# Kernel tuning notes

Measured on AMD Instinct MI355X. Metric: run time of the kernel, lower is better.

The kernel has to match this reference:

```python
import jax, jax.numpy as jnp
import numpy as np

K = 5            # neighbors
TEMP = 1.0       # softmax temperature
BANK = 1000      # fixed bank capacity in source
B = 65536        # batch
D = 256          # feature_dim
EPS = 1e-12      # F.normalize eps


def _l2norm(x):
    # F.normalize(x, dim=1): x / max(||x||, eps)
    n = jnp.sqrt(jnp.sum(x * x, axis=1, keepdims=True))
    return x / jnp.maximum(n, EPS)


def setup_inputs() -> dict:
    key = jax.random.key(0)
    k1, k2, k3, k4 = jax.random.split(key, 4)
    features = jax.random.normal(k1, (B, D), dtype=jnp.float32)
    feature_bank = jax.random.normal(k2, (BANK, D), dtype=jnp.float32)
    # fusion_layer: Linear(2D -> D), ReLU, Linear(D -> D). torch weight layout [out, in].
    W1 = jax.random.normal(k3, (D, 2 * D), dtype=jnp.float32) * (1.0 / np.sqrt(2 * D))
    b1 = jnp.zeros((D,), dtype=jnp.float32)
    W2 = jax.random.normal(k4, (D, D), dtype=jnp.float32) * (1.0 / np.sqrt(D))
    b2 = jnp.zeros((D,), dtype=jnp.float32)
    return {"features": features, "feature_bank": feature_bank,
            "W1": W1, "b1": b1, "W2": W2, "b2": b2}


def reference(features, feature_bank, W1, b1, W2, b2):
    # knn_search: cosine similarity against the (full) bank
    qn = _l2norm(features)                      # [B, D]
    bn = _l2norm(feature_bank)                  # [BANK, D]
    sims = qn @ bn.T                            # [B, BANK]
    top_s, top_i = jax.lax.top_k(sims, K)       # [B, K]
    w = jax.nn.softmax(top_s / TEMP, axis=1)    # [B, K]
    neigh = feature_bank[top_i]                 # gather -> [B, K, D]
    nf = jnp.einsum('bkd,bk->bd', neigh, w)     # weighted average of neighbors
    # fusion MLP on concat([query, neighbors])
    fused = jnp.concatenate([features, nf], axis=1)    # [B, 2D]
    h = jax.nn.relu(fused @ W1.T + b1)                 # [B, D]
    out = h @ W2.T + b2                                # [B, D]
    return out
```

## Files before the change

### kernel.cpp

```cpp
#include <hip/hip_runtime.h>

#define DIM 256
#define NC 12

typedef __attribute__((ext_vector_type(8))) short short8;
typedef __attribute__((ext_vector_type(4))) float f32x4;

__device__ __forceinline__ short f32bf(float f) {
    unsigned u = __builtin_bit_cast(unsigned, f);
    unsigned r = u + 0x7FFFu + ((u >> 16) & 1u);
    return (short)(r >> 16);
}

__device__ __forceinline__ void gld_lds16(const void* g, void* l) {
    __builtin_amdgcn_global_load_lds((const __attribute__((address_space(1))) unsigned int*)g,
                                     (__attribute__((address_space(3))) unsigned int*)l, 16, 0, 0);
}

template<int CTRL>
__device__ __forceinline__ unsigned dppmax(unsigned x) {
    unsigned y = (unsigned)__builtin_amdgcn_update_dpp(0, (int)x, CTRL, 0xF, 0xF, true);
    return x > y ? x : y;
}

__global__ __launch_bounds__(256) void k_prep(const float* __restrict__ bank,
        const float* __restrict__ W1, const float* __restrict__ W2,
        short* __restrict__ bnbf, double* __restrict__ binv,
        short* __restrict__ w1bf, short* __restrict__ w2bf)
{
    __shared__ double part[4];
    __shared__ double s_inv;
    const int bid = blockIdx.x, t = threadIdx.x;
    if (bid < 1024) {
        const int row = bid;
        if (row < 1000) {
            float v = bank[(size_t)row * DIM + t];
            double ssq = (double)v * (double)v;
            for (int o = 32; o > 0; o >>= 1) ssq += __shfl_down(ssq, o);
            if ((t & 63) == 0) part[t >> 6] = ssq;
            __syncthreads();
            if (t == 0) {
                double s = part[0] + part[1] + part[2] + part[3];
                double n = sqrt(s); if (n < 1e-12) n = 1e-12;
                double inv = 1.0 / n;
                binv[row] = inv; s_inv = inv;
            }
            __syncthreads();
            const int pcol = (((t >> 3) ^ (row & 7)) << 3) | (t & 7);
            bnbf[(size_t)row * DIM + pcol] = f32bf((float)((double)v * s_inv));
        } else {
            bnbf[(size_t)row * DIM + t] = 0;
            if (t == 0) binv[row] = 0.0;
        }
    } else if (bid < 1536) {
        const int i = (bid - 1024) * 256 + t;
        w1bf[i] = f32bf(W1[i]);
    } else {
        const int i = (bid - 1536) * 256 + t;
        w2bf[i] = f32bf(W2[i]);
    }
}

__global__ __launch_bounds__(256) void k_sims(const float* __restrict__ feat,
        const short* __restrict__ bnbf, short* __restrict__ sims, int qoff)
{
    __shared__ alignas(16) short Qs[32 * 264];
    __shared__ alignas(16) short Ab[64 * 256];
    const int t = threadIdx.x, lane = t & 63, w = t >> 6;
    const int n16 = lane & 15, q4 = lane >> 4;

    {
        const int r = t >> 3, p = t & 7;
        const float4* src = (const float4*)(feat + (size_t)(qoff + blockIdx.x * 32 + r) * DIM + p * 32);
        short* dst = Qs + r * 264 + p * 32;
        #pragma unroll
        for (int i = 0; i < 8; ++i) {
            float4 v = src[i];
            dst[i*4+0] = f32bf(v.x); dst[i*4+1] = f32bf(v.y);
            dst[i*4+2] = f32bf(v.z); dst[i*4+3] = f32bf(v.w);
        }
    }
    const char* gA = (const char*)bnbf;
    char* lA = (char*)Ab;
    #pragma unroll
    for (int i = 0; i < 8; ++i)
        gld_lds16(gA + i * 4096 + t * 16, lA + i * 4096 + (t >> 6) * 1024);
    __syncthreads();

    short8 bq[8][2];
    #pragma unroll
    for (int kc = 0; kc < 8; ++kc)
        #pragma unroll
        for (int nt = 0; nt < 2; ++nt)
            bq[kc][nt] = *(const short8*)(Qs + (nt * 16 + n16) * 264 + kc * 32 + q4 * 8);

    const int ml = w * 16 + n16;
    int aoff[8];
    #pragma unroll
    for (int kc = 0; kc < 8; ++kc)
        aoff[kc] = (ml * 256 + (((kc * 4 + q4) ^ (ml & 7)) << 3)) * 2;

    const f32x4 vzero = {0.f, 0.f, 0.f, 0.f};
    for (int chunk = 0; chunk < 16; ++chunk) {
        f32x4 acc[2];
        acc[0] = vzero; acc[1] = vzero;
        #pragma unroll
        for (int kc = 0; kc < 8; ++kc) {
            short8 af = *(const short8*)(lA + aoff[kc]);
            #pragma unroll
            for (int nt = 0; nt < 2; ++nt)
                acc[nt] = __builtin_amdgcn_mfma_f32_16x16x32_bf16(af, bq[kc][nt], acc[nt], 0, 0, 0);
        }
        const int bankb = chunk * 64 + w * 16 + q4 * 4;
        #pragma unroll
        for (int nt = 0; nt < 2; ++nt) {
            const int qc = blockIdx.x * 32 + nt * 16 + n16;
            uint2 u;
            u.x = ((unsigned)(unsigned short)f32bf(acc[nt][0])) |
                  (((unsigned)(unsigned short)f32bf(acc[nt][1])) << 16);
            u.y = ((unsigned)(unsigned short)f32bf(acc[nt][2])) |
                  (((unsigned)(unsigned short)f32bf(acc[nt][3])) << 16);
            *(uint2*)(sims + (size_t)qc * 1024 + bankb) = u;
        }
        __syncthreads();
        if (chunk < 15) {
            #pragma unroll
            for (int i = 0; i < 8; ++i)
                gld_lds16(gA + (size_t)(chunk + 1) * 32768 + i * 4096 + t * 16,
                          lA + i * 4096 + (t >> 6) * 1024);
            __syncthreads();
        }
    }
}

__global__ __launch_bounds__(256) void k_select(const short* __restrict__ sims,
        int* __restrict__ top, int qoff)
{
    const int t = threadIdx.x, lane = t & 63, w = t >> 6;
    const int q = blockIdx.x * 4 + w;
    const uint4* p = (const uint4*)(sims + (size_t)q * 1024 + lane * 16);
    uint4 a = p[0], b = p[1];

    unsigned k[16];
    {
        unsigned words[8] = {a.x, a.y, a.z, a.w, b.x, b.y, b.z, b.w};
        #pragma unroll
        for (int j = 0; j < 16; ++j) {
            unsigned h = (j & 1) ? (words[j >> 1] >> 16) : (words[j >> 1] & 0xFFFFu);
            unsigned m = (h ^ 0x8000u) ^ ((0u - (h >> 15)) & 0x7FFFu);
            int idx = lane * 16 + j;
            k[j] = (idx < 1000) ? ((m << 16) | (unsigned)idx) : 0u;
        }
    }
    #pragma unroll
    for (int sz = 2; sz <= 16; sz <<= 1)
        #pragma unroll
        for (int st = sz >> 1; st >= 1; st >>= 1)
            #pragma unroll
            for (int i = 0; i < 16; ++i) {
                int j = i ^ st;
                if (j > i) {
                    bool desc = ((i & sz) == 0);
                    unsigned lo = k[i], hi = k[j];
                    unsigned mx = lo > hi ? lo : hi;
                    unsigned mn = lo > hi ? hi : lo;
                    k[i] = desc ? mx : mn;
                    k[j] = desc ? mn : mx;
                }
            }
    unsigned mine = 0;
    #pragma unroll
    for (int r = 0; r < 12; ++r) {
        unsigned m = k[0];
        m = dppmax<0xB1>(m);
        m = dppmax<0x4E>(m);
        m = dppmax<0x141>(m);
        m = dppmax<0x140>(m);
        m = dppmax<0x142>(m);
        m = dppmax<0x143>(m);
        unsigned wm = (unsigned)__builtin_amdgcn_readlane((int)m, 63);
        if (lane == r) mine = wm;
        if (k[0] == wm) {
            #pragma unroll
            for (int s = 0; s < 12; ++s) k[s] = k[s + 1];
        }
    }
    if (lane < 12) top[(size_t)(qoff + q) * NC + lane] = (int)(mine & 0xFFFFu);
}

__global__ __launch_bounds__(256) void k_refine(const float* __restrict__ feat,
        const float* __restrict__ bank, const int* __restrict__ top,
        const double* __restrict__ binv, short* __restrict__ nf)
{
    __shared__ int    cidxL[16 * NC];
    __shared__ float  bdF[16 * NC];
    __shared__ double bdD[16 * NC];
    __shared__ float  simsF[16 * NC];
    __shared__ double simsD[16 * NC];
    __shared__ float  qiL[16];
    __shared__ int    flagL[16];
    __shared__ int    selidx[16][5];
    __shared__ float  selw[16][5];

    const int t = threadIdx.x, lane = t & 63, w = t >> 6;
    const int g = lane >> 4, u = lane & 15;
    const int ql = w * 4 + g;
    const int qbase = blockIdx.x * 16;
    const int q = qbase + ql;

    if (t < 16 * NC) {
        const int c = top[(size_t)qbase * NC + t];
        cidxL[t] = c;
        const double b = binv[c];
        bdD[t] = b; bdF[t] = (float)b;
    }
    __syncthreads();

    int ci[NC];
    #pragma unroll
    for (int c = 0; c < NC; ++c) ci[c] = cidxL[ql * NC + c];

    float qf[16];
    float ssf = 0.f;
    #pragma unroll
    for (int j = 0; j < 4; ++j) {
        float4 v = *(const float4*)(feat + (size_t)q * DIM + j * 64 + u * 4);
        qf[j*4+0] = v.x; qf[j*4+1] = v.y; qf[j*4+2] = v.z; qf[j*4+3] = v.w;
        ssf += v.x*v.x + v.y*v.y + v.z*v.z + v.w*v.w;
    }
    #pragma unroll
    for (int o = 1; o < 16; o <<= 1) ssf += __shfl_xor(ssf, o, 16);
    float nq = sqrtf(ssf); if (nq < 1e-12f) nq = 1e-12f;
    if (u == 0) qiL[ql] = 1.f / nq;

    float s[NC];
    #pragma unroll
    for (int c = 0; c < NC; ++c) {
        const float* brow = bank + (size_t)ci[c] * DIM + u * 4;
        float a0 = 0.f, a1 = 0.f, a2 = 0.f, a3 = 0.f;
        #pragma unroll
        for (int j = 0; j < 4; ++j) {
            float4 b = *(const float4*)(brow + j * 64);
            a0 += qf[j*4+0] * b.x; a1 += qf[j*4+1] * b.y;
            a2 += qf[j*4+2] * b.z; a3 += qf[j*4+3] * b.w;
        }
        s[c] = (a0 + a1) + (a2 + a3);
    }
    #pragma unroll
    for (int o = 1; o < 16; o <<= 1)
        #pragma unroll
        for (int c = 0; c < NC; ++c) s[c] += __shfl_xor(s[c], o, 16);
    #pragma unroll
    for (int c = 0; c < NC; ++c) if (u == c) simsF[ql * NC + c] = s[c];
    __syncthreads();

    if (t < 16) {
        const float qi2 = qiL[t];
        float vf[NC];
        unsigned long long key[NC];
        int cid[NC];
        #pragma unroll
        for (int c = 0; c < NC; ++c) {
            cid[c] = cidxL[t * NC + c];
            float v = simsF[t * NC + c] * qi2 * bdF[t * NC + c];
            vf[c] = v;
            unsigned ub = __builtin_bit_cast(unsigned, v);
            unsigned m = (ub >> 31) ? ~ub : (ub | 0x80000000u);
            key[c] = ((unsigned long long)m << 10) | (unsigned long long)(1023 - cid[c]);
        }
        int rank[NC];
        #pragma unroll
        for (int c = 0; c < NC; ++c) rank[c] = 0;
        #pragma unroll
        for (int c1 = 0; c1 < NC; ++c1)
            #pragma unroll
            for (int c2 = c1 + 1; c2 < NC; ++c2) {
                const bool gt = key[c1] > key[c2];
                rank[c2] += gt ? 1 : 0;
                rank[c1] += gt ? 0 : 1;
            }
        float v5 = 0.f, v6 = 0.f;
        #pragma unroll
        for (int c = 0; c < NC; ++c) {
            v5 += (rank[c] == 4) ? vf[c] : 0.f;
            v6 += (rank[c] == 5) ? vf[c] : 0.f;
        }
        flagL[t] = (v5 - v6) < 2e-6f;

        float vm = vf[0];
        #pragma unroll
        for (int c = 1; c < NC; ++c) vm = fmaxf(vm, vf[c]);
        float e[NC]; float wsum = 0.f;
        #pragma unroll
        for (int c = 0; c < NC; ++c) {
            float ex = __expf(vf[c] - vm);
            ex = (rank[c] < 5) ? ex : 0.f;
            e[c] = ex; wsum += ex;
        }
        const float inv = 1.f / wsum;
        #pragma unroll
        for (int k = 0; k < 5; ++k) {
            int idx = 0; float wv = 0.f;
            #pragma unroll
            for (int c = 0; c < NC; ++c) {
                const bool is = (rank[c] == k);
                idx += is ? cid[c] : 0;
                wv  += is ? e[c]  : 0.f;
            }
            selidx[t][k] = idx; selw[t][k] = wv * inv;
        }
    }
    __syncthreads();

    if (flagL[ql]) {
        double ssd = 0.0;
        #pragma unroll
        for (int j = 0; j < 16; ++j) ssd += (double)qf[j] * (double)qf[j];
        #pragma unroll
        for (int o = 1; o < 16; o <<= 1) ssd += __shfl_xor(ssd, o, 16);
        double nd = sqrt(ssd); if (nd < 1e-12) nd = 1e-12;
        const double qid = 1.0 / nd;
        double sd[NC];
        #pragma unroll
        for (int c = 0; c < NC; ++c) {
            const float* brow = bank + (size_t)ci[c] * DIM + u * 4;
            double a0 = 0, a1 = 0, a2 = 0, a3 = 0;
            #pragma unroll
            for (int j = 0; j < 4; ++j) {
                float4 b = *(const float4*)(brow + j * 64);
                a0 += (double)qf[j*4+0] * b.x; a1 += (double)qf[j*4+1] * b.y;
                a2 += (double)qf[j*4+2] * b.z; a3 += (double)qf[j*4+3] * b.w;
            }
            sd[c] = (a0 + a1) + (a2 + a3);
        }
        #pragma unroll
        for (int o = 1; o < 16; o <<= 1)
            #pragma unroll
            for (int c = 0; c < NC; ++c) sd[c] += __shfl_xor(sd[c], o, 16);
        #pragma unroll
        for (int c = 0; c < NC; ++c)
            if (u == c) simsD[ql * NC + c] = sd[c] * qid * bdD[ql * NC + c];
    }
    __syncthreads();

    if (t < 16 && flagL[t]) {
        double vd[NC];
        unsigned long long key[NC];
        int cid[NC];
        #pragma unroll
        for (int c = 0; c < NC; ++c) {
            cid[c] = cidxL[t * NC + c];
            double v = simsD[t * NC + c];
            vd[c] = v;
            unsigned long long ub = __builtin_bit_cast(unsigned long long, v);
            unsigned long long m = (ub >> 63) ? ~ub : (ub | 0x8000000000000000ULL);
            key[c] = (m & ~0x3FFULL) | (unsigned long long)(1023 - cid[c]);
        }
        int rank[NC];
        #pragma unroll
        for (int c = 0; c < NC; ++c) rank[c] = 0;
        #pragma unroll
        for (int c1 = 0; c1 < NC; ++c1)
            #pragma unroll
            for (int c2 = c1 + 1; c2 < NC; ++c2) {
                const bool gt = key[c1] > key[c2];
                rank[c2] += gt ? 1 : 0;
                rank[c1] += gt ? 0 : 1;
            }
        float vf[NC];
        #pragma unroll
        for (int c = 0; c < NC; ++c) vf[c] = (float)vd[c];
        float vm = vf[0];
        #pragma unroll
        for (int c = 1; c < NC; ++c) vm = fmaxf(vm, vf[c]);
        float e[NC]; float wsum = 0.f;
        #pragma unroll
        for (int c = 0; c < NC; ++c) {
            float ex = __expf(vf[c] - vm);
            ex = (rank[c] < 5) ? ex : 0.f;
            e[c] = ex; wsum += ex;
        }
        const float inv = 1.f / wsum;
        #pragma unroll
        for (int k = 0; k < 5; ++k) {
            int idx = 0; float wv = 0.f;
            #pragma unroll
            for (int c = 0; c < NC; ++c) {
                const bool is = (rank[c] == k);
                idx += is ? cid[c] : 0;
                wv  += is ? e[c]  : 0.f;
            }
            selidx[t][k] = idx; selw[t][k] = wv * inv;
        }
    }
    __syncthreads();

    float wk[5]; int ik[5];
    #pragma unroll
    for (int k = 0; k < 5; ++k) { wk[k] = selw[ql][k]; ik[k] = selidx[ql][k]; }
    float4 oa[4];
    #pragma unroll
    for (int j = 0; j < 4; ++j) { oa[j].x = 0.f; oa[j].y = 0.f; oa[j].z = 0.f; oa[j].w = 0.f; }
    #pragma unroll
    for (int k = 0; k < 5; ++k) {
        const float wc = wk[k];
        const float* brow = bank + (size_t)ik[k] * DIM + u * 4;
        #pragma unroll
        for (int j = 0; j < 4; ++j) {
            float4 b = *(const float4*)(brow + j * 64);
            oa[j].x += wc * b.x; oa[j].y += wc * b.y;
            oa[j].z += wc * b.z; oa[j].w += wc * b.w;
        }
    }
    short* od = nf + (size_t)q * DIM + u * 4;
    #pragma unroll
    for (int j = 0; j < 4; ++j) {
        uint2 pk;
        pk.x = ((unsigned)(unsigned short)f32bf(oa[j].x)) |
               (((unsigned)(unsigned short)f32bf(oa[j].y)) << 16);
        pk.y = ((unsigned)(unsigned short)f32bf(oa[j].z)) |
               (((unsigned)(unsigned short)f32bf(oa[j].w)) << 16);
        *(uint2*)(od + j * 64) = pk;
    }
}

__global__ __launch_bounds__(256, 4) void k_mlp(const float* __restrict__ feat,
        const short* __restrict__ nf, const short* __restrict__ w1bf,
        const short* __restrict__ w2bf, const float* __restrict__ b1,
        const float* __restrict__ b2, float* __restrict__ out)
{
    __shared__ alignas(16) short As[2][64 * 40];
    __shared__ alignas(16) short Hs[64 * 264];
    const int t = threadIdx.x, lane = t & 63, w = t >> 6;
    const int mb = blockIdx.x * 64;
    const int r = t >> 2, p = t & 3;
    const int n16 = lane & 15, ko = (lane >> 4) << 3;
    const int rq = (lane >> 4) << 2, cc = lane & 15;
    const f32x4 vzero = {0.f, 0.f, 0.f, 0.f};

    f32x4 acc[4][4];
    #pragma unroll
    for (int a = 0; a < 4; ++a)
        #pragma unroll
        for (int b = 0; b < 4; ++b) acc[a][b] = vzero;

    {
        const float4* s = (const float4*)(feat + (size_t)(mb + r) * 256 + p * 8);
        float4 v0 = s[0], v1 = s[1];
        short* ad = As[0] + r * 40 + p * 8;
        ad[0] = f32bf(v0.x); ad[1] = f32bf(v0.y); ad[2] = f32bf(v0.z); ad[3] = f32bf(v0.w);
        ad[4] = f32bf(v1.x); ad[5] = f32bf(v1.y); ad[6] = f32bf(v1.z); ad[7] = f32bf(v1.w);
    }
    __syncthreads();

    for (int kc = 0; kc < 16; ++kc) {
        if (kc < 15) {
            const int kn = kc + 1;
            short* ad = As[kn & 1] + r * 40 + p * 8;
            if (kn < 8) {
                const float4* s = (const float4*)(feat + (size_t)(mb + r) * 256 + kn * 32 + p * 8);
                float4 v0 = s[0], v1 = s[1];
                ad[0] = f32bf(v0.x); ad[1] = f32bf(v0.y); ad[2] = f32bf(v0.z); ad[3] = f32bf(v0.w);
                ad[4] = f32bf(v1.x); ad[5] = f32bf(v1.y); ad[6] = f32bf(v1.z); ad[7] = f32bf(v1.w);
            } else {
                *(uint4*)ad = *(const uint4*)(nf + (size_t)(mb + r) * 256 + (kn - 8) * 32 + p * 8);
            }
        }
        short8 bf[4];
        #pragma unroll
        for (int nt = 0; nt < 4; ++nt)
            bf[nt] = *(const short8*)(w1bf + (size_t)(w * 64 + nt * 16 + n16) * 512 + kc * 32 + ko);
        short8 af[4];
        const short* cur = As[kc & 1];
        #pragma unroll
        for (int mt = 0; mt < 4; ++mt)
            af[mt] = *(const short8*)(cur + (mt * 16 + n16) * 40 + ko);
        #pragma unroll
        for (int mt = 0; mt < 4; ++mt)
            #pragma unroll
            for (int nt = 0; nt < 4; ++nt)
                acc[mt][nt] = __builtin_amdgcn_mfma_f32_16x16x32_bf16(af[mt], bf[nt], acc[mt][nt], 0, 0, 0);
        __syncthreads();
    }

    #pragma unroll
    for (int mt = 0; mt < 4; ++mt)
        #pragma unroll
        for (int nt = 0; nt < 4; ++nt) {
            const int row = mt * 16 + rq;
            const int col = w * 64 + nt * 16 + cc;
            const float bias = b1[col];
            #pragma unroll
            for (int rr = 0; rr < 4; ++rr) {
                float v = acc[mt][nt][rr] + bias;
                Hs[(row + rr) * 264 + col] = f32bf(fmaxf(v, 0.f));
            }
        }
    #pragma unroll
    for (int a = 0; a < 4; ++a)
        #pragma unroll
        for (int b = 0; b < 4; ++b) acc[a][b] = vzero;
    __syncthreads();

    for (int kc = 0; kc < 8; ++kc) {
        short8 bf[4];
        #pragma unroll
        for (int nt = 0; nt < 4; ++nt)
            bf[nt] = *(const short8*)(w2bf + (size_t)(w * 64 + nt * 16 + n16) * 256 + kc * 32 + ko);
        short8 af[4];
        #pragma unroll
        for (int mt = 0; mt < 4; ++mt)
            af[mt] = *(const short8*)(Hs + (mt * 16 + n16) * 264 + kc * 32 + ko);
        #pragma unroll
        for (int mt = 0; mt < 4; ++mt)
            #pragma unroll
            for (int nt = 0; nt < 4; ++nt)
                acc[mt][nt] = __builtin_amdgcn_mfma_f32_16x16x32_bf16(af[mt], bf[nt], acc[mt][nt], 0, 0, 0);
    }
    #pragma unroll
    for (int mt = 0; mt < 4; ++mt)
        #pragma unroll
        for (int nt = 0; nt < 4; ++nt) {
            const int row = mb + mt * 16 + rq;
            const int col = w * 64 + nt * 16 + cc;
            const float bias = b2[col];
            #pragma unroll
            for (int rr = 0; rr < 4; ++rr)
                out[(size_t)(row + rr) * 256 + col] = acc[mt][nt][rr] + bias;
        }
}

extern "C" void kernel_launch(void* const* d_in, const int* in_sizes, int n_in,
                              void* d_out, int out_size, void* d_ws, size_t ws_size,
                              hipStream_t stream) {
    const float* feat = (const float*)d_in[0];
    const float* bank = (const float*)d_in[1];
    const float* W1   = (const float*)d_in[2];
    const float* b1   = (const float*)d_in[3];
    const float* W2   = (const float*)d_in[4];
    const float* b2   = (const float*)d_in[5];
    float* out = (float*)d_out;

    char* ws = (char*)d_ws;
    short*  bnbf = (short*)(ws + 0);
    double* binv = (double*)(ws + 524288);
    short*  w1bf = (short*)(ws + 532480);
    short*  w2bf = (short*)(ws + 794624);
    int*    top  = (int*)(ws + 925696);
    short*  nf   = (short*)(ws + 4071424);
    short*  X    = (short*)(ws + 37625856);

    k_prep<<<1792, 256, 0, stream>>>(bank, W1, W2, bnbf, binv, w1bf, w2bf);
    for (int s = 0; s < 4; ++s) {
        const int qoff = s * 16384;
        k_sims  <<<512,  256, 0, stream>>>(feat, bnbf, X, qoff);
        k_select<<<4096, 256, 0, stream>>>(X, top, qoff);
    }
    k_refine<<<4096, 256, 0, stream>>>(feat, bank, top, binv, nf);
    k_mlp   <<<1024, 256, 0, stream>>>(feat, nf, w1bf, w2bf, b1, b2, out);
}
```

Baseline: 385.0 us.

## Emit bf16 features in refine and feed MLP fragments directly from global memory

```diff
diff --git a/kernel.cpp b/kernel.cpp
--- a/kernel.cpp
+++ b/kernel.cpp
@@ -190,7 +190,8 @@
 
 __global__ __launch_bounds__(256) void k_refine(const float* __restrict__ feat,
         const float* __restrict__ bank, const int* __restrict__ top,
-        const double* __restrict__ binv, short* __restrict__ nf)
+        const double* __restrict__ binv, short* __restrict__ nf,
+        short* __restrict__ featbf)
 {
     __shared__ int    cidxL[16 * NC];
     __shared__ float  bdF[16 * NC];
@@ -228,6 +229,18 @@
         qf[j*4+0] = v.x; qf[j*4+1] = v.y; qf[j*4+2] = v.z; qf[j*4+3] = v.w;
         ssf += v.x*v.x + v.y*v.y + v.z*v.z + v.w*v.w;
     }
+    {
+        short* fb = featbf + (size_t)q * DIM + u * 4;
+        #pragma unroll
+        for (int j = 0; j < 4; ++j) {
+            uint2 pk;
+            pk.x = ((unsigned)(unsigned short)f32bf(qf[j*4+0])) |
+                   (((unsigned)(unsigned short)f32bf(qf[j*4+1])) << 16);
+            pk.y = ((unsigned)(unsigned short)f32bf(qf[j*4+2])) |
+                   (((unsigned)(unsigned short)f32bf(qf[j*4+3])) << 16);
+            *(uint2*)(fb + j * 64) = pk;
+        }
+    }
     #pragma unroll
     for (int o = 1; o < 16; o <<= 1) ssf += __shfl_xor(ssf, o, 16);
     float nq = sqrtf(ssf); if (nq < 1e-12f) nq = 1e-12f;
@@ -424,16 +437,14 @@
     }
 }
 
-__global__ __launch_bounds__(256, 4) void k_mlp(const float* __restrict__ feat,
+__global__ __launch_bounds__(256, 4) void k_mlp(const short* __restrict__ featbf,
         const short* __restrict__ nf, const short* __restrict__ w1bf,
         const short* __restrict__ w2bf, const float* __restrict__ b1,
         const float* __restrict__ b2, float* __restrict__ out)
 {
-    __shared__ alignas(16) short As[2][64 * 40];
     __shared__ alignas(16) short Hs[64 * 264];
     const int t = threadIdx.x, lane = t & 63, w = t >> 6;
     const int mb = blockIdx.x * 64;
-    const int r = t >> 2, p = t & 3;
     const int n16 = lane & 15, ko = (lane >> 4) << 3;
     const int rq = (lane >> 4) << 2, cc = lane & 15;
     const f32x4 vzero = {0.f, 0.f, 0.f, 0.f};
@@ -444,43 +455,39 @@
         #pragma unroll
         for (int b = 0; b < 4; ++b) acc[a][b] = vzero;
 
-    {
-        const float4* s = (const float4*)(feat + (size_t)(mb + r) * 256 + p * 8);
-        float4 v0 = s[0], v1 = s[1];
-        short* ad = As[0] + r * 40 + p * 8;
-        ad[0] = f32bf(v0.x); ad[1] = f32bf(v0.y); ad[2] = f32bf(v0.z); ad[3] = f32bf(v0.w);
-        ad[4] = f32bf(v1.x); ad[5] = f32bf(v1.y); ad[6] = f32bf(v1.z); ad[7] = f32bf(v1.w);
-    }
-    __syncthreads();
-
-    for (int kc = 0; kc < 16; ++kc) {
-        if (kc < 15) {
-            const int kn = kc + 1;
-            short* ad = As[kn & 1] + r * 40 + p * 8;
-            if (kn < 8) {
-                const float4* s = (const float4*)(feat + (size_t)(mb + r) * 256 + kn * 32 + p * 8);
-                float4 v0 = s[0], v1 = s[1];
-                ad[0] = f32bf(v0.x); ad[1] = f32bf(v0.y); ad[2] = f32bf(v0.z); ad[3] = f32bf(v0.w);
-                ad[4] = f32bf(v1.x); ad[5] = f32bf(v1.y); ad[6] = f32bf(v1.z); ad[7] = f32bf(v1.w);
-            } else {
-                *(uint4*)ad = *(const uint4*)(nf + (size_t)(mb + r) * 256 + (kn - 8) * 32 + p * 8);
-            }
-        }
-        short8 bf[4];
+    const short* A0 = featbf + (size_t)mb * 256 + ko;
+    const short* A1 = nf     + (size_t)mb * 256 + ko;
+    const short* Wp = w1bf + (size_t)(w * 64 + n16) * 512 + ko;
+
+    #pragma unroll
+    for (int kc = 0; kc < 8; ++kc) {
+        short8 af[4], bf[4];
+        #pragma unroll
+        for (int mt = 0; mt < 4; ++mt)
+            af[mt] = *(const short8*)(A0 + (mt * 16 + n16) * 256 + kc * 32);
         #pragma unroll
         for (int nt = 0; nt < 4; ++nt)
-            bf[nt] = *(const short8*)(w1bf + (size_t)(w * 64 + nt * 16 + n16) * 512 + kc * 32 + ko);
-        short8 af[4];
-        const short* cur = As[kc & 1];
-        #pragma unroll
-        for (int mt = 0; mt < 4; ++mt)
-            af[mt] = *(const short8*)(cur + (mt * 16 + n16) * 40 + ko);
+            bf[nt] = *(const short8*)(Wp + (size_t)nt * 16 * 512 + kc * 32);
         #pragma unroll
         for (int mt = 0; mt < 4; ++mt)
             #pragma unroll
             for (int nt = 0; nt < 4; ++nt)
                 acc[mt][nt] = __builtin_amdgcn_mfma_f32_16x16x32_bf16(af[mt], bf[nt], acc[mt][nt], 0, 0, 0);
-        __syncthreads();
+    }
+    #pragma unroll
+    for (int kc = 0; kc < 8; ++kc) {
+        short8 af[4], bf[4];
+        #pragma unroll
+        for (int mt = 0; mt < 4; ++mt)
+            af[mt] = *(const short8*)(A1 + (mt * 16 + n16) * 256 + kc * 32);
+        #pragma unroll
+        for (int nt = 0; nt < 4; ++nt)
+            bf[nt] = *(const short8*)(Wp + (size_t)nt * 16 * 512 + (kc + 8) * 32);
+        #pragma unroll
+        for (int mt = 0; mt < 4; ++mt)
+            #pragma unroll
+            for (int nt = 0; nt < 4; ++nt)
+                acc[mt][nt] = __builtin_amdgcn_mfma_f32_16x16x32_bf16(af[mt], bf[nt], acc[mt][nt], 0, 0, 0);
     }
 
     #pragma unroll
@@ -502,6 +509,7 @@
         for (int b = 0; b < 4; ++b) acc[a][b] = vzero;
     __syncthreads();
 
+    #pragma unroll
     for (int kc = 0; kc < 8; ++kc) {
         short8 bf[4];
         #pragma unroll
@@ -549,6 +557,7 @@
     int*    top  = (int*)(ws + 925696);
     short*  nf   = (short*)(ws + 4071424);
     short*  X    = (short*)(ws + 37625856);
+    short*  featbf = X;
 
     k_prep<<<1792, 256, 0, stream>>>(bank, W1, W2, bnbf, binv, w1bf, w2bf);
     for (int s = 0; s < 4; ++s) {
@@ -556,6 +565,6 @@
         k_sims  <<<512,  256, 0, stream>>>(feat, bnbf, X, qoff);
         k_select<<<4096, 256, 0, stream>>>(X, top, qoff);
     }
-    k_refine<<<4096, 256, 0, stream>>>(feat, bank, top, binv, nf);
-    k_mlp   <<<1024, 256, 0, stream>>>(feat, nf, w1bf, w2bf, b1, b2, out);
-}
+    k_refine<<<4096, 256, 0, stream>>>(feat, bank, top, binv, nf, featbf);
+    k_mlp   <<<1024, 256, 0, stream>>>(featbf, nf, w1bf, w2bf, b1, b2, out);
+}
```

Result: slower. 397.0 us (+3.1%).
